# Optimization experiments

Measured on AMD Instinct MI355X. Metric: run time of the kernel, lower is better.

## Reference

```python
import jax, jax.numpy as jnp
import numpy as np

NUM_HEADS = 16
THETA = 10000.0

def _rope(t, token_ids, theta):
    # t: [B, H, S, Dk]; token_ids: [S]
    d_k = t.shape[-1]
    inv_freq = theta ** (-jnp.arange(0, d_k, 2, dtype=jnp.float32) / d_k)  # [Dk/2]
    ang = token_ids.astype(jnp.float32)[:, None] * inv_freq[None, :]       # [S, Dk/2]
    cos, sin = jnp.cos(ang), jnp.sin(ang)
    x1, x2 = t[..., ::2], t[..., 1::2]
    r1 = x1 * cos - x2 * sin
    r2 = x1 * sin + x2 * cos
    return jnp.stack([r1, r2], axis=-1).reshape(t.shape)

def setup_inputs() -> dict:
    key = jax.random.key(0)
    ks = jax.random.split(key, 5)
    d_model = 1024
    scale = 0.02
    return {
        "x": jax.random.normal(ks[0], (4, 2048, d_model), dtype=jnp.float32),
        "token_ids": jnp.arange(2048, dtype=jnp.int32),
        "Wq": jax.random.normal(ks[1], (d_model, d_model), dtype=jnp.float32) * scale,
        "Wk": jax.random.normal(ks[2], (d_model, d_model), dtype=jnp.float32) * scale,
        "Wv": jax.random.normal(ks[3], (d_model, d_model), dtype=jnp.float32) * scale,
        "Wo": jax.random.normal(ks[4], (d_model, d_model), dtype=jnp.float32) * scale,
    }

def reference(x, token_ids, Wq, Wk, Wv, Wo):
    B, S, D = x.shape
    H = NUM_HEADS
    Dk = D // H
    def split_heads(t):
        return t.reshape(B, S, H, Dk).transpose(0, 2, 1, 3)  # [B,H,S,Dk]
    q = split_heads(x @ Wq.T)
    k = split_heads(x @ Wk.T)
    v = split_heads(x @ Wv.T)
    q = _rope(q, token_ids, THETA)
    k = _rope(k, token_ids, THETA)
    scores = jnp.einsum("bhqd,bhkd->bhqk", q, k) / jnp.sqrt(jnp.float32(Dk))
    causal = jnp.tril(jnp.ones((S, S), dtype=bool))
    scores = jnp.where(causal, scores, jnp.float32(-1e9))
    attn = jax.nn.softmax(scores, axis=-1)
    out = jnp.einsum("bhqk,bhkd->bhqd", attn, v)
    out = out.transpose(0, 2, 1, 3).reshape(B, S, H * Dk)
    return out @ Wo.T
```

## Files before the change

### kernel.cpp

```cpp
#include <hip/hip_runtime.h>

#define BATCH 4
#define SLEN 2048
#define DMODEL 1024
#define NHEADS 16
#define DK 64
#define MROWS (BATCH * SLEN)
#define NQB 16
#define SCALE_LOG2E 0.1803368801111731f

typedef short bf16x8 __attribute__((ext_vector_type(8)));
typedef unsigned short u16x4 __attribute__((ext_vector_type(4)));
typedef float f32x4 __attribute__((ext_vector_type(4)));

__device__ __forceinline__ unsigned short f2bf(float f) {
    unsigned u = __float_as_uint(f);
    unsigned r = u + 0x7FFFu + ((u >> 16) & 1u);
    return (unsigned short)(r >> 16);
}

__device__ __forceinline__ void gload_lds16(const void* g, void* l) {
    __builtin_amdgcn_global_load_lds(
        (const __attribute__((address_space(1))) void*)g,
        (__attribute__((address_space(3))) void*)l, 16, 0, 0);
}

__global__ void cvt_f32_bf16(const float* __restrict__ in, unsigned short* __restrict__ out, int n) {
    int i = (blockIdx.x * blockDim.x + threadIdx.x) * 4;
    if (i >= n) return;
    float4 v = *reinterpret_cast<const float4*>(in + i);
    u16x4 o;
    o[0] = f2bf(v.x); o[1] = f2bf(v.y); o[2] = f2bf(v.z); o[3] = f2bf(v.w);
    *reinterpret_cast<u16x4*>(out + i) = o;
}

__global__ void rope_table(const int* __restrict__ tok, float* __restrict__ cs, float* __restrict__ sn) {
    int idx = blockIdx.x * blockDim.x + threadIdx.x;
    if (idx >= SLEN * 32) return;
    int s = idx >> 5, fi = idx & 31;
    float invf = powf(10000.0f, -(float)(2 * fi) / 64.0f);
    float ang = (float)tok[s] * invf;
    cs[idx] = cosf(ang);
    sn[idx] = sinf(ang);
}

__device__ __forceinline__ void gemm128_core(
    const unsigned short* __restrict__ A, const unsigned short* __restrict__ B,
    int m0, int n0, int tid, f32x4 (&acc)[4][4],
    unsigned short* As, unsigned short* Bs)
{
    int lane = tid & 63, wave = tid >> 6;
    int ln = lane & 15, kq = lane >> 4;
    int wr = wave >> 1, wc = wave & 1;
#pragma unroll
    for (int a = 0; a < 4; a++)
#pragma unroll
        for (int b = 0; b < 4; b++) acc[a][b] = (f32x4){0.f, 0.f, 0.f, 0.f};

    for (int k0 = 0; k0 < DMODEL; k0 += 64) {
        if (k0) __syncthreads();
#pragma unroll
        for (int i = 0; i < 4; i++) {
            int s = i * 256 + tid;
            int r = s >> 3;
            int u = (s & 7) ^ (r & 7);
            gload_lds16(A + (size_t)(m0 + r) * DMODEL + k0 + u * 8, &As[(i * 256 + wave * 64) * 8]);
            gload_lds16(B + (size_t)(n0 + r) * DMODEL + k0 + u * 8, &Bs[(i * 256 + wave * 64) * 8]);
        }
        __syncthreads();

        bf16x8 af[4][2], bfr[4][2];
#pragma unroll
        for (int mt = 0; mt < 4; mt++) {
            int row = wr * 64 + mt * 16 + ln;
#pragma unroll
            for (int kc = 0; kc < 2; kc++) {
                int u = (kc * 4 + kq) ^ (row & 7);
                af[mt][kc] = *reinterpret_cast<const bf16x8*>(&As[row * 64 + u * 8]);
            }
        }
#pragma unroll
        for (int nt = 0; nt < 4; nt++) {
            int row = wc * 64 + nt * 16 + ln;
#pragma unroll
            for (int kc = 0; kc < 2; kc++) {
                int u = (kc * 4 + kq) ^ (row & 7);
                bfr[nt][kc] = *reinterpret_cast<const bf16x8*>(&Bs[row * 64 + u * 8]);
            }
        }
        __builtin_amdgcn_s_setprio(1);
#pragma unroll
        for (int kc = 0; kc < 2; kc++)
#pragma unroll
            for (int mt = 0; mt < 4; mt++)
#pragma unroll
                for (int nt = 0; nt < 4; nt++)
                    acc[mt][nt] = __builtin_amdgcn_mfma_f32_16x16x32_bf16(af[mt][kc], bfr[nt][kc], acc[mt][nt], 0, 0, 0);
        __builtin_amdgcn_s_setprio(0);
    }
}

__global__ __launch_bounds__(256) void qkv_gemm(
    const unsigned short* __restrict__ X,
    const unsigned short* __restrict__ Wq,
    const unsigned short* __restrict__ Wk,
    const unsigned short* __restrict__ Wv,
    const float* __restrict__ cs_tab, const float* __restrict__ sn_tab,
    unsigned short* __restrict__ Q, unsigned short* __restrict__ K,
    unsigned short* __restrict__ VT)
{
    __shared__ alignas(16) unsigned short As[128 * 64];
    __shared__ alignas(16) unsigned short Bs[128 * 64];
    int tid = threadIdx.x, lane = tid & 63, wave = tid >> 6;
    int ln = lane & 15, kq = lane >> 4;
    int wr = wave >> 1, wc = wave & 1;
    int m0 = blockIdx.x * 128;
    int n0 = blockIdx.y * 128;
    int z = blockIdx.z;
    const unsigned short* W = (z == 0) ? Wq : (z == 1) ? Wk : Wv;

    f32x4 acc[4][4];
    gemm128_core(X, W, m0, n0, tid, acc, As, Bs);

    bool isV = (z == 2);
    bool isQ = (z == 0);
    unsigned short* dstQK = (z == 0) ? Q : K;
    int m0w = m0 + wr * 64, n0w = n0 + wc * 64;
#pragma unroll
    for (int nt = 0; nt < 4; nt++) {
        int n = n0w + nt * 16 + ln;
        int h = n >> 6, d = n & 63;
        int fi = d >> 1;
#pragma unroll
        for (int mt = 0; mt < 4; mt++) {
#pragma unroll
            for (int j = 0; j < 4; j++) {
                int m = m0w + mt * 16 + kq * 4 + j;
                int b = m >> 11, s = m & (SLEN - 1);
                float v = acc[mt][nt][j];
                if (!isV) {
                    float c = cs_tab[s * 32 + fi];
                    float si = sn_tab[s * 32 + fi];
                    float p = __shfl_xor(v, 1);
                    v = (d & 1) ? (p * si + v * c) : (v * c - p * si);
                    if (isQ) v *= SCALE_LOG2E;
                    dstQK[(((size_t)(b * NHEADS + h) * SLEN + s) << 6) + d] = f2bf(v);
                } else {
                    VT[((size_t)(b * NHEADS + h) * DK + d) * SLEN + s] = f2bf(v);
                }
            }
        }
    }
}

__global__ __launch_bounds__(256) void attn_kernel(
    const unsigned short* __restrict__ Q, const unsigned short* __restrict__ K,
    const unsigned short* __restrict__ VT, unsigned short* __restrict__ O)
{
    __shared__ alignas(16) unsigned short Kt[2][4096];
    __shared__ alignas(16) unsigned short Vt[2][4096];
    __shared__ alignas(16) unsigned short P_lds[4][32][72];

    int tid = threadIdx.x, lane = tid & 63, wave = tid >> 6;
    int ln = lane & 15, kq = lane >> 4;
    int qb = blockIdx.x;
    int h = blockIdx.y, b = blockIdx.z;
    size_t headoff = ((size_t)b * NHEADS + h) * SLEN * DK;
    const unsigned short* Qh = Q + headoff;
    const unsigned short* Kh = K + headoff;
    const unsigned short* Vh = VT + headoff;

    auto stage = [&](int buf, int t) {
        int kv0 = t << 6;
#pragma unroll
        for (int i = 0; i < 2; i++) {
            int s = i * 256 + tid;
            int r = s >> 3;
            int cb = (s & 7) ^ (r & 7);
            gload_lds16(Kh + (size_t)(kv0 + r) * DK + cb * 8,
                        &Kt[buf][(i * 256 + wave * 64) * 8]);
            gload_lds16(Vh + (size_t)r * SLEN + kv0 + cb * 8,
                        &Vt[buf][(i * 256 + wave * 64) * 8]);
        }
    };

    for (int sid = 0; sid < 2; sid++) {
        int qs = sid ? qb : (NQB - 1 - qb);
        int q0 = qs * 128 + wave * 32;

        bf16x8 aq[2][2];
#pragma unroll
        for (int mt = 0; mt < 2; mt++)
#pragma unroll
            for (int kc = 0; kc < 2; kc++)
                aq[mt][kc] = *reinterpret_cast<const bf16x8*>(
                    Qh + (size_t)(q0 + mt * 16 + ln) * DK + kc * 32 + kq * 8);

        f32x4 oacc[2][4];
#pragma unroll
        for (int mt = 0; mt < 2; mt++)
#pragma unroll
            for (int nt = 0; nt < 4; nt++) oacc[mt][nt] = (f32x4){0.f, 0.f, 0.f, 0.f};
        float m_r[2] = {-1e30f, -1e30f};
        float l_r[2] = {0.f, 0.f};

        int tmax_w = (q0 + 31) >> 6;
        int ntiles = 2 * qs + 2;

        stage(0, 0);
        __syncthreads();

        for (int t = 0; t < ntiles; t++) {
            int buf = t & 1;
            if (t + 1 < ntiles) stage(buf ^ 1, t + 1);

            if (t <= tmax_w) {
                int kv0 = t << 6;
                f32x4 sacc[2][4];
#pragma unroll
                for (int mt = 0; mt < 2; mt++)
#pragma unroll
                    for (int nt = 0; nt < 4; nt++) sacc[mt][nt] = (f32x4){0.f, 0.f, 0.f, 0.f};
                __builtin_amdgcn_s_setprio(1);
#pragma unroll
                for (int nt = 0; nt < 4; nt++) {
                    int rr = nt * 16 + ln;
#pragma unroll
                    for (int kc = 0; kc < 2; kc++) {
                        int unit = (kc * 4 + kq) ^ (rr & 7);
                        bf16x8 bk = *reinterpret_cast<const bf16x8*>(&Kt[buf][rr * 64 + unit * 8]);
#pragma unroll
                        for (int mt = 0; mt < 2; mt++)
                            sacc[mt][nt] = __builtin_amdgcn_mfma_f32_16x16x32_bf16(bk, aq[mt][kc], sacc[mt][nt], 0, 0, 0);
                    }
                }
                __builtin_amdgcn_s_setprio(0);

                if (kv0 + 63 > q0) {
#pragma unroll
                    for (int mt = 0; mt < 2; mt++) {
                        int q = q0 + mt * 16 + ln;
#pragma unroll
                        for (int nt = 0; nt < 4; nt++)
#pragma unroll
                            for (int j = 0; j < 4; j++) {
                                int k = kv0 + nt * 16 + kq * 4 + j;
                                if (k > q) sacc[mt][nt][j] = -1e30f;
                            }
                    }
                }

                float mloc[2];
#pragma unroll
                for (int mt = 0; mt < 2; mt++) {
                    f32x4 m4 = sacc[mt][0];
#pragma unroll
                    for (int nt = 1; nt < 4; nt++) {
                        m4[0] = fmaxf(m4[0], sacc[mt][nt][0]);
                        m4[1] = fmaxf(m4[1], sacc[mt][nt][1]);
                        m4[2] = fmaxf(m4[2], sacc[mt][nt][2]);
                        m4[3] = fmaxf(m4[3], sacc[mt][nt][3]);
                    }
                    mloc[mt] = fmaxf(fmaxf(m4[0], m4[1]), fmaxf(m4[2], m4[3]));
                }
#pragma unroll
                for (int mt = 0; mt < 2; mt++) {
                    mloc[mt] = fmaxf(mloc[mt], __shfl_xor(mloc[mt], 16));
                    mloc[mt] = fmaxf(mloc[mt], __shfl_xor(mloc[mt], 32));
                }

                bool needscale = !__all((mloc[0] <= m_r[0] + 8.0f) && (mloc[1] <= m_r[1] + 8.0f));
                float so[2] = {1.f, 1.f};
                if (needscale) {
#pragma unroll
                    for (int mt = 0; mt < 2; mt++) {
                        float mn = fmaxf(m_r[mt], mloc[mt]);
                        so[mt] = exp2f(m_r[mt] - mn);
                        m_r[mt] = mn;
                    }
                }

                float rs[2] = {0.f, 0.f};
#pragma unroll
                for (int mt = 0; mt < 2; mt++)
#pragma unroll
                    for (int nt = 0; nt < 4; nt++)
#pragma unroll
                        for (int j = 0; j < 4; j++) {
                            float p = exp2f(sacc[mt][nt][j] - m_r[mt]);
                            sacc[mt][nt][j] = p;
                            rs[mt] += p;
                        }
#pragma unroll
                for (int mt = 0; mt < 2; mt++) {
                    rs[mt] += __shfl_xor(rs[mt], 16);
                    rs[mt] += __shfl_xor(rs[mt], 32);
                    l_r[mt] = l_r[mt] * so[mt] + rs[mt];
                }

                if (needscale) {
                    float so_o[2][4];
#pragma unroll
                    for (int mt = 0; mt < 2; mt++)
#pragma unroll
                        for (int j = 0; j < 4; j++)
                            so_o[mt][j] = __shfl(so[mt], kq * 4 + j, 16);
#pragma unroll
                    for (int mt = 0; mt < 2; mt++)
#pragma unroll
                        for (int nt = 0; nt < 4; nt++)
#pragma unroll
                            for (int j = 0; j < 4; j++)
                                oacc[mt][nt][j] *= so_o[mt][j];
                }

#pragma unroll
                for (int mt = 0; mt < 2; mt++)
#pragma unroll
                    for (int nt = 0; nt < 4; nt++) {
                        u16x4 o;
#pragma unroll
                        for (int j = 0; j < 4; j++) o[j] = f2bf(sacc[mt][nt][j]);
                        *reinterpret_cast<u16x4*>(&P_lds[wave][mt * 16 + ln][nt * 16 + kq * 4]) = o;
                    }
                asm volatile("s_waitcnt lgkmcnt(0)" ::: "memory");
                __builtin_amdgcn_sched_barrier(0);

                bf16x8 pa[2][2];
#pragma unroll
                for (int mt = 0; mt < 2; mt++)
#pragma unroll
                    for (int kc = 0; kc < 2; kc++)
                        pa[mt][kc] = *reinterpret_cast<const bf16x8*>(&P_lds[wave][mt * 16 + ln][kc * 32 + kq * 8]);

                __builtin_amdgcn_s_setprio(1);
#pragma unroll
                for (int nt = 0; nt < 4; nt++) {
                    int rr = nt * 16 + ln;
#pragma unroll
                    for (int kc = 0; kc < 2; kc++) {
                        int unit = (kc * 4 + kq) ^ (rr & 7);
                        bf16x8 bv = *reinterpret_cast<const bf16x8*>(&Vt[buf][rr * 64 + unit * 8]);
#pragma unroll
                        for (int mt = 0; mt < 2; mt++)
                            oacc[mt][nt] = __builtin_amdgcn_mfma_f32_16x16x32_bf16(pa[mt][kc], bv, oacc[mt][nt], 0, 0, 0);
                    }
                }
                __builtin_amdgcn_s_setprio(0);
            }
            __syncthreads();
        }

        float lo[2][4];
#pragma unroll
        for (int mt = 0; mt < 2; mt++)
#pragma unroll
            for (int j = 0; j < 4; j++)
                lo[mt][j] = __shfl(l_r[mt], kq * 4 + j, 16);
#pragma unroll
        for (int mt = 0; mt < 2; mt++)
#pragma unroll
            for (int nt = 0; nt < 4; nt++)
#pragma unroll
                for (int j = 0; j < 4; j++) {
                    int row = q0 + mt * 16 + kq * 4 + j;
                    float v = oacc[mt][nt][j] / lo[mt][j];
                    O[((size_t)b * SLEN + row) * DMODEL + h * 64 + nt * 16 + ln] = f2bf(v);
                }
        __syncthreads();
    }
}

__global__ __launch_bounds__(256) void out_gemm(
    const unsigned short* __restrict__ A, const unsigned short* __restrict__ Wo,
    float* __restrict__ out)
{
    __shared__ alignas(16) unsigned short As[128 * 64];
    __shared__ alignas(16) unsigned short Bs[128 * 64];
    int tid = threadIdx.x, lane = tid & 63, wave = tid >> 6;
    int ln = lane & 15, kq = lane >> 4;
    int wr = wave >> 1, wc = wave & 1;
    int m0 = blockIdx.x * 128;
    int n0 = blockIdx.y * 128;

    f32x4 acc[4][4];
    gemm128_core(A, Wo, m0, n0, tid, acc, As, Bs);

    int m0w = m0 + wr * 64, n0w = n0 + wc * 64;
#pragma unroll
    for (int mt = 0; mt < 4; mt++)
#pragma unroll
        for (int nt = 0; nt < 4; nt++)
#pragma unroll
            for (int j = 0; j < 4; j++) {
                int m = m0w + mt * 16 + kq * 4 + j;
                int n = n0w + nt * 16 + ln;
                out[(size_t)m * DMODEL + n] = acc[mt][nt][j];
            }
}

extern "C" void kernel_launch(void* const* d_in, const int* in_sizes, int n_in,
                              void* d_out, int out_size, void* d_ws, size_t ws_size,
                              hipStream_t stream) {
    const float* x  = (const float*)d_in[0];
    const int* tok  = (const int*)d_in[1];
    const float* wq = (const float*)d_in[2];
    const float* wk = (const float*)d_in[3];
    const float* wv = (const float*)d_in[4];
    const float* wo = (const float*)d_in[5];
    float* out = (float*)d_out;

    const size_t XB_OFF = 0;
    const size_t WQ_OFF = 16777216;
    const size_t WK_OFF = 18874368;
    const size_t WV_OFF = 20971520;
    const size_t WO_OFF = 23068672;
    const size_t Q_OFF  = 25165824;
    const size_t K_OFF  = 41943040;
    const size_t VT_OFF = 58720256;
    const size_t O_OFF  = 75497472;
    const size_t CS_OFF = 92274688;
    const size_t SN_OFF = 92536832;
    const size_t WS_NEEDED = 92798976;
    if (ws_size < WS_NEEDED) return;

    char* ws = (char*)d_ws;
    unsigned short* Xb  = (unsigned short*)(ws + XB_OFF);
    unsigned short* Wqb = (unsigned short*)(ws + WQ_OFF);
    unsigned short* Wkb = (unsigned short*)(ws + WK_OFF);
    unsigned short* Wvb = (unsigned short*)(ws + WV_OFF);
    unsigned short* Wob = (unsigned short*)(ws + WO_OFF);
    unsigned short* Qb  = (unsigned short*)(ws + Q_OFF);
    unsigned short* Kb  = (unsigned short*)(ws + K_OFF);
    unsigned short* VTb = (unsigned short*)(ws + VT_OFF);
    unsigned short* Ob  = (unsigned short*)(ws + O_OFF);
    float* cs_tab = (float*)(ws + CS_OFF);
    float* sn_tab = (float*)(ws + SN_OFF);

    cvt_f32_bf16<<<8192, 256, 0, stream>>>(x,  Xb,  MROWS * DMODEL);
    cvt_f32_bf16<<<1024, 256, 0, stream>>>(wq, Wqb, DMODEL * DMODEL);
    cvt_f32_bf16<<<1024, 256, 0, stream>>>(wk, Wkb, DMODEL * DMODEL);
    cvt_f32_bf16<<<1024, 256, 0, stream>>>(wv, Wvb, DMODEL * DMODEL);
    cvt_f32_bf16<<<1024, 256, 0, stream>>>(wo, Wob, DMODEL * DMODEL);
    rope_table<<<256, 256, 0, stream>>>(tok, cs_tab, sn_tab);

    qkv_gemm<<<dim3(MROWS / 128, DMODEL / 128, 3), 256, 0, stream>>>(
        Xb, Wqb, Wkb, Wvb, cs_tab, sn_tab, Qb, Kb, VTb);

    attn_kernel<<<dim3(SLEN / 256, NHEADS, BATCH), 256, 0, stream>>>(Qb, Kb, VTb, Ob);

    out_gemm<<<dim3(MROWS / 128, DMODEL / 128, 1), 256, 0, stream>>>(Ob, Wob, out);
}
```

Before: 231.2 us.

## Keep softmax P in registers via permuted K row layout; merge weight conversions

K rows are loaded into LDS in a permuted order, so the S accumulator layout from the QK MFMA lines up with the A-operand layout of the PV MFMA. The P tile can then be packed straight into bf16x8 registers with v_cvt_pk_bf16_f32, with no round trip through LDS and no waitcnt. The causal mask index is updated to match the permutation. The P_lds buffer is removed and launch bounds now request 4 blocks per CU, and the four weight conversion launches are merged into one kernel to cut launch overhead. The risks are a wrong permutation breaking correctness and register pressure under the tighter launch bound.

Result: faster. 214.6 us (-7.2%).

```diff
diff --git a/kernel.cpp b/kernel.cpp
--- a/kernel.cpp
+++ b/kernel.cpp
@@ -19,6 +19,12 @@
     return (unsigned short)(r >> 16);
 }
 
+__device__ __forceinline__ unsigned pkbf(float a, float b) {
+    unsigned r;
+    asm volatile("v_cvt_pk_bf16_f32 %0, %1, %2" : "=v"(r) : "v"(a), "v"(b));
+    return r;
+}
+
 __device__ __forceinline__ void gload_lds16(const void* g, void* l) {
     __builtin_amdgcn_global_load_lds(
         (const __attribute__((address_space(1))) void*)g,
@@ -32,6 +38,20 @@
     u16x4 o;
     o[0] = f2bf(v.x); o[1] = f2bf(v.y); o[2] = f2bf(v.z); o[3] = f2bf(v.w);
     *reinterpret_cast<u16x4*>(out + i) = o;
+}
+
+__global__ void cvt_w_all(const float* __restrict__ w0, const float* __restrict__ w1,
+                          const float* __restrict__ w2, const float* __restrict__ w3,
+                          unsigned short* __restrict__ o0, unsigned short* __restrict__ o1,
+                          unsigned short* __restrict__ o2, unsigned short* __restrict__ o3) {
+    int z = blockIdx.y;
+    const float* src = (z == 0) ? w0 : (z == 1) ? w1 : (z == 2) ? w2 : w3;
+    unsigned short* dst = (z == 0) ? o0 : (z == 1) ? o1 : (z == 2) ? o2 : o3;
+    int i = (blockIdx.x * blockDim.x + threadIdx.x) * 4;
+    float4 v = *reinterpret_cast<const float4*>(src + i);
+    u16x4 o;
+    o[0] = f2bf(v.x); o[1] = f2bf(v.y); o[2] = f2bf(v.z); o[3] = f2bf(v.w);
+    *reinterpret_cast<u16x4*>(dst + i) = o;
 }
 
 __global__ void rope_table(const int* __restrict__ tok, float* __restrict__ cs, float* __restrict__ sn) {
@@ -153,13 +173,12 @@
     }
 }
 
-__global__ __launch_bounds__(256) void attn_kernel(
+__global__ __launch_bounds__(256, 4) void attn_kernel(
     const unsigned short* __restrict__ Q, const unsigned short* __restrict__ K,
     const unsigned short* __restrict__ VT, unsigned short* __restrict__ O)
 {
     __shared__ alignas(16) unsigned short Kt[2][4096];
     __shared__ alignas(16) unsigned short Vt[2][4096];
-    __shared__ alignas(16) unsigned short P_lds[4][32][72];
 
     int tid = threadIdx.x, lane = tid & 63, wave = tid >> 6;
     int ln = lane & 15, kq = lane >> 4;
@@ -177,7 +196,8 @@
             int s = i * 256 + tid;
             int r = s >> 3;
             int cb = (s & 7) ^ (r & 7);
-            gload_lds16(Kh + (size_t)(kv0 + r) * DK + cb * 8,
+            int rp = ((r >> 5) << 5) | (((r >> 2) & 3) << 3) | (((r >> 4) & 1) << 2) | (r & 3);
+            gload_lds16(Kh + (size_t)(kv0 + rp) * DK + cb * 8,
                         &Kt[buf][(i * 256 + wave * 64) * 8]);
             gload_lds16(Vh + (size_t)r * SLEN + kv0 + cb * 8,
                         &Vt[buf][(i * 256 + wave * 64) * 8]);
@@ -244,7 +264,7 @@
                         for (int nt = 0; nt < 4; nt++)
 #pragma unroll
                             for (int j = 0; j < 4; j++) {
-                                int k = kv0 + nt * 16 + kq * 4 + j;
+                                int k = kv0 + (nt >> 1) * 32 + kq * 8 + (nt & 1) * 4 + j;
                                 if (k > q) sacc[mt][nt][j] = -1e30f;
                             }
                     }
@@ -314,24 +334,18 @@
                                 oacc[mt][nt][j] *= so_o[mt][j];
                 }
 
+                bf16x8 pa[2][2];
 #pragma unroll
                 for (int mt = 0; mt < 2; mt++)
 #pragma unroll
-                    for (int nt = 0; nt < 4; nt++) {
-                        u16x4 o;
-#pragma unroll
-                        for (int j = 0; j < 4; j++) o[j] = f2bf(sacc[mt][nt][j]);
-                        *reinterpret_cast<u16x4*>(&P_lds[wave][mt * 16 + ln][nt * 16 + kq * 4]) = o;
-                    }
-                asm volatile("s_waitcnt lgkmcnt(0)" ::: "memory");
-                __builtin_amdgcn_sched_barrier(0);
-
-                bf16x8 pa[2][2];
-#pragma unroll
-                for (int mt = 0; mt < 2; mt++)
-#pragma unroll
-                    for (int kc = 0; kc < 2; kc++)
-                        pa[mt][kc] = *reinterpret_cast<const bf16x8*>(&P_lds[wave][mt * 16 + ln][kc * 32 + kq * 8]);
+                    for (int kc = 0; kc < 2; kc++) {
+                        union { unsigned u[4]; bf16x8 v; } r;
+                        r.u[0] = pkbf(sacc[mt][2 * kc][0], sacc[mt][2 * kc][1]);
+                        r.u[1] = pkbf(sacc[mt][2 * kc][2], sacc[mt][2 * kc][3]);
+                        r.u[2] = pkbf(sacc[mt][2 * kc + 1][0], sacc[mt][2 * kc + 1][1]);
+                        r.u[3] = pkbf(sacc[mt][2 * kc + 1][2], sacc[mt][2 * kc + 1][3]);
+                        pa[mt][kc] = r.v;
+                    }
 
                 __builtin_amdgcn_s_setprio(1);
 #pragma unroll
@@ -437,11 +451,8 @@
     float* cs_tab = (float*)(ws + CS_OFF);
     float* sn_tab = (float*)(ws + SN_OFF);
 
-    cvt_f32_bf16<<<8192, 256, 0, stream>>>(x,  Xb,  MROWS * DMODEL);
-    cvt_f32_bf16<<<1024, 256, 0, stream>>>(wq, Wqb, DMODEL * DMODEL);
-    cvt_f32_bf16<<<1024, 256, 0, stream>>>(wk, Wkb, DMODEL * DMODEL);
-    cvt_f32_bf16<<<1024, 256, 0, stream>>>(wv, Wvb, DMODEL * DMODEL);
-    cvt_f32_bf16<<<1024, 256, 0, stream>>>(wo, Wob, DMODEL * DMODEL);
+    cvt_f32_bf16<<<8192, 256, 0, stream>>>(x, Xb, MROWS * DMODEL);
+    cvt_w_all<<<dim3(1024, 4), 256, 0, stream>>>(wq, wk, wv, wo, Wqb, Wkb, Wvb, Wob);
     rope_table<<<256, 256, 0, stream>>>(tok, cs_tab, sn_tab);
 
     qkv_gemm<<<dim3(MROWS / 128, DMODEL / 128, 3), 256, 0, stream>>>(
```
